# Kernel optimization log

Hardware: AMD Instinct MI355X
Metric: run time of the kernel (lower is better)

The kernel has to match this reference:

```python
import jax, jax.numpy as jnp
import numpy as np

R_MAX = 32
S_MAX = 2
DIM_OUT = 128
N_R = 2 * R_MAX + 2            # 66 bins for rel_pos / rel_token
N_S = 2 * S_MAX + 2            # 6 bins for rel_chain
DIM_IN = 2 * N_R + 1 + N_S     # 139 packed feature dim: [rel_pos|rel_token|mask|rel_chain]


def setup_inputs() -> dict:
    key = jax.random.key(0)
    # LinearNoBias weight, torch convention: y = x @ W.T, W: (dim_out, dim_in)
    W = jax.random.normal(key, (DIM_OUT, DIM_IN), dtype=jnp.float32) * 0.02
    return {"batch_size": 1, "seq_len": 1024, "W": W}


def reference(batch_size, seq_len, W):
    # token_idx = arange(seq_len) (no chain breaks => complex_chain_break_indices is None)
    tok = jnp.arange(seq_len)
    diff = tok[:, None] - tok[None, :]                      # (n, n) = i - j
    # d_token = clip(diff + r_max, 0, 2*r_max); onehot bins = arange(66).
    # argmin |v - arange(66)| == v for integer v in [0, 64], so the one-hot
    # index is exactly the clipped value (embedding-gather form of the
    # original onehot + dense matmul).
    bucket = jnp.clip(diff + R_MAX, 0, 2 * R_MAX)           # (n, n) int
    # d_res is constant r_max -> one-hot index r_max in rel_pos block.
    # mask_same_entity is constant 1.
    # d_chain is constant 2*s_max+1 -> one-hot index 2*s_max+1 in rel_chain block.
    W_pos = W[:, :N_R]                                      # (dim_out, 66)
    W_token = W[:, N_R:2 * N_R]                             # (dim_out, 66)
    w_mask = W[:, 2 * N_R]                                  # (dim_out,)
    W_chain = W[:, 2 * N_R + 1:]                            # (dim_out, 6)
    const = W_pos[:, R_MAX] + w_mask + W_chain[:, 2 * S_MAX + 1]  # (dim_out,)
    out = jnp.take(W_token.T, bucket, axis=0) + const       # (n, n, dim_out)
    return jnp.broadcast_to(out[None], (batch_size, seq_len, seq_len, DIM_OUT))
```

## Files before the change

kernel.cpp:

```cpp
#include <hip/hip_runtime.h>

#define R_MAX 32
#define DIM_OUT 128
#define N_R 66
#define DIM_IN 139

typedef float f32x4 __attribute__((ext_vector_type(4)));

__global__ __launch_bounds__(256) void rpe_kernel(const int* __restrict__ p_seq,
                                                  const float* __restrict__ W,
                                                  f32x4* __restrict__ out,
                                                  unsigned long long n_rows) {
    const unsigned seq = (unsigned)*p_seq;
    const unsigned tid = threadIdx.x;
    const unsigned lane = tid & 31;
    const float* w0 = W + (size_t)(lane * 4) * DIM_IN;

    float cst[4];
    f32x4 vhi, vlo;
    #pragma unroll
    for (int k = 0; k < 4; ++k) {
        const float* w = w0 + (size_t)k * DIM_IN;
        cst[k] = (w[R_MAX] + w[2 * N_R]) + w[DIM_IN - 1];
        vhi[k] = w[N_R + 2 * R_MAX] + cst[k];
        vlo[k] = w[N_R + 0] + cst[k];
    }

    const unsigned n_irows = (unsigned)(n_rows / seq);
    const unsigned CPR = 2;
    const unsigned total_chunks = n_irows * CPR;

    for (unsigned chunk = blockIdx.x; chunk < total_chunks; chunk += gridDim.x) {
        const unsigned irow = chunk / CPR;
        const unsigned half = chunk - irow * CPR;
        const int i = (int)(irow % seq);
        const int j0 = (int)((half * seq) / CPR);
        const int j1 = (int)(((half + 1) * seq) / CPR);

        int e1 = i - 31; e1 = e1 < j0 ? j0 : (e1 > j1 ? j1 : e1);
        int e2 = i + 32; e2 = e2 < j0 ? j0 : (e2 > j1 ? j1 : e2);

        f32x4* __restrict__ base = out + (size_t)irow * seq * (DIM_OUT / 4);

        for (int f = j0 * 32 + (int)tid; f < e1 * 32; f += 256)
            base[f] = vhi;

        for (int f = e1 * 32 + (int)tid; f < e2 * 32; f += 256) {
            const int j = f >> 5;
            const int b = i - j + R_MAX;
            f32x4 v;
            v[0] = w0[0 * DIM_IN + N_R + b] + cst[0];
            v[1] = w0[1 * DIM_IN + N_R + b] + cst[1];
            v[2] = w0[2 * DIM_IN + N_R + b] + cst[2];
            v[3] = w0[3 * DIM_IN + N_R + b] + cst[3];
            base[f] = v;
        }

        for (int f = e2 * 32 + (int)tid; f < j1 * 32; f += 256)
            base[f] = vlo;
    }
}

extern "C" void kernel_launch(void* const* d_in, const int* in_sizes, int n_in,
                              void* d_out, int out_size, void* d_ws, size_t ws_size,
                              hipStream_t stream) {
    const int* p_seq = (const int*)d_in[1];
    const float* W = (const float*)d_in[2];
    f32x4* out = (f32x4*)d_out;

    const unsigned long long n_rows = (unsigned long long)out_size / DIM_OUT;

    rpe_kernel<<<2048, 256, 0, stream>>>(p_seq, W, out, n_rows);
}
```

Baseline: 102.3 us.

## Replace per-row chunk loops with flat grid-stride loop over output vectors

Swaps the per-row chunking, where each block writes half a row in three segments (constant high, band, constant low), for a flat grid-stride loop over every float4 of the output. The (i, j) indices are advanced incrementally with carry arithmetic, so no per-iteration divisions are needed, and each element picks vlo, vhi or a gathered band value through a branch. The aim is more uniform work distribution and fully regular coalesced stores with no per-segment loop overhead. In exchange, every element now pays a clamp and a branch, and a wave that straddles the band boundary diverges.

```diff
diff --git a/kernel.cpp b/kernel.cpp
--- a/kernel.cpp
+++ b/kernel.cpp
@@ -10,7 +10,7 @@
 __global__ __launch_bounds__(256) void rpe_kernel(const int* __restrict__ p_seq,
                                                   const float* __restrict__ W,
                                                   f32x4* __restrict__ out,
-                                                  unsigned long long n_rows) {
+                                                  unsigned long long n_vec) {
     const unsigned seq = (unsigned)*p_seq;
     const unsigned tid = threadIdx.x;
     const unsigned lane = tid & 31;
@@ -26,38 +26,38 @@
         vlo[k] = w[N_R + 0] + cst[k];
     }
 
-    const unsigned n_irows = (unsigned)(n_rows / seq);
-    const unsigned CPR = 2;
-    const unsigned total_chunks = n_irows * CPR;
+    const unsigned G = gridDim.x * 256u;
+    unsigned long long v = (unsigned long long)blockIdx.x * 256u + tid;
 
-    for (unsigned chunk = blockIdx.x; chunk < total_chunks; chunk += gridDim.x) {
-        const unsigned irow = chunk / CPR;
-        const unsigned half = chunk - irow * CPR;
-        const int i = (int)(irow % seq);
-        const int j0 = (int)((half * seq) / CPR);
-        const int j1 = (int)(((half + 1) * seq) / CPR);
+    const unsigned djf = G >> 5;
+    const unsigned jf0 = (unsigned)(v >> 5);
+    unsigned j = jf0 % seq;
+    unsigned i = (jf0 / seq) % seq;
+    const unsigned dj = djf % seq;
+    const unsigned di = (djf / seq) % seq;
 
-        int e1 = i - 31; e1 = e1 < j0 ? j0 : (e1 > j1 ? j1 : e1);
-        int e2 = i + 32; e2 = e2 < j0 ? j0 : (e2 > j1 ? j1 : e2);
+    for (; v < n_vec; v += G) {
+        int b = (int)i - (int)j + R_MAX;
+        b = b < 0 ? 0 : (b > 2 * R_MAX ? 2 * R_MAX : b);
 
-        f32x4* __restrict__ base = out + (size_t)irow * seq * (DIM_OUT / 4);
+        f32x4 val;
+        if (b == 0) {
+            val = vlo;
+        } else if (b == 2 * R_MAX) {
+            val = vhi;
+        } else {
+            val[0] = w0[0 * DIM_IN + N_R + b] + cst[0];
+            val[1] = w0[1 * DIM_IN + N_R + b] + cst[1];
+            val[2] = w0[2 * DIM_IN + N_R + b] + cst[2];
+            val[3] = w0[3 * DIM_IN + N_R + b] + cst[3];
+        }
+        out[v] = val;
 
-        for (int f = j0 * 32 + (int)tid; f < e1 * 32; f += 256)
-            base[f] = vhi;
-
-        for (int f = e1 * 32 + (int)tid; f < e2 * 32; f += 256) {
-            const int j = f >> 5;
-            const int b = i - j + R_MAX;
-            f32x4 v;
-            v[0] = w0[0 * DIM_IN + N_R + b] + cst[0];
-            v[1] = w0[1 * DIM_IN + N_R + b] + cst[1];
-            v[2] = w0[2 * DIM_IN + N_R + b] + cst[2];
-            v[3] = w0[3 * DIM_IN + N_R + b] + cst[3];
-            base[f] = v;
-        }
-
-        for (int f = e2 * 32 + (int)tid; f < j1 * 32; f += 256)
-            base[f] = vlo;
+        j += dj;
+        unsigned c = (j >= seq) ? 1u : 0u;
+        j -= c ? seq : 0u;
+        i += di + c;
+        if (i >= seq) i -= seq;
     }
 }
 
@@ -68,7 +68,7 @@
     const float* W = (const float*)d_in[2];
     f32x4* out = (f32x4*)d_out;
 
-    const unsigned long long n_rows = (unsigned long long)out_size / DIM_OUT;
+    const unsigned long long n_vec = (unsigned long long)out_size / 4;
 
-    rpe_kernel<<<2048, 256, 0, stream>>>(p_seq, W, out, n_rows);
+    rpe_kernel<<<2048, 256, 0, stream>>>(p_seq, W, out, n_vec);
 }
```

Result: slower. 113.1 us (+10.5%).
